# Kernel optimization log

Hardware: AMD Instinct MI355X
Metric: run time of the kernel (lower is better)

## Reference

```python
import jax, jax.numpy as jnp
import numpy as np
from jax.scipy.special import logsumexp

B, D, A = 64, 128, 128


def setup_inputs() -> dict:
    key = jax.random.key(0)
    k1, k2, k3, k4 = jax.random.split(key, 4)
    x = jax.random.randint(k1, (B, D), 0, 2).astype(jnp.float32)  # binary observations
    u_log_p_a1 = jax.random.normal(k2, (1, 1, 1, A), dtype=jnp.float32)
    u_log_transition = jax.random.normal(k3, (D - 1, A, A), dtype=jnp.float32)
    log_p_xi_g_ai = jax.random.normal(k4, (1, D, 1, A), dtype=jnp.float32)
    return {
        "x": x,
        "u_log_p_a1": u_log_p_a1,
        "u_log_transition": u_log_transition,
        "log_p_xi_g_ai": log_p_xi_g_ai,
    }


def reference(x, u_log_p_a1, u_log_transition, log_p_xi_g_ai):
    b, d = x.shape
    a = u_log_p_a1.shape[-1]
    # _normalize_logits == log_softmax along last dim
    log_p_a1 = jax.nn.log_softmax(u_log_p_a1, axis=-1)          # [1,1,1,A]
    log_T = jax.nn.log_softmax(u_log_transition, axis=-1)        # [D-1,A,A]
    # Bernoulli(logits=l).log_prob(v) = v*l - softplus(l)
    l = log_p_xi_g_ai                                            # [1,D,1,A]
    log_px_vec = x[:, :, None, None] * l - jax.nn.softplus(l)    # [B,D,1,A]
    # per-step reduction matrices
    red = log_px_vec[:, 1:] + log_T                              # [B,D-1,A,A]
    # initial matrix: row-repeated initial vector
    init = jnp.broadcast_to(log_px_vec[:, 0] + log_p_a1[0], (b, a, a))  # [B,A,A]
    mats = jnp.transpose(red, (1, 0, 2, 3))                      # [D-1,B,A,A]

    def step(M, T):
        # log-space matmul: new[b,i,j] = logsumexp_k M[b,i,k] + T[b,k,j]
        new = logsumexp(M[:, :, :, None] + T[:, None, :, :], axis=2)
        return new, None

    final, _ = jax.lax.scan(step, init, mats)                    # [B,A,A]
    log_px = logsumexp(final, axis=-1)                           # [B,A] (rows identical)
    return (log_px, log_p_a1)
```

## Files before the change

kernel.cpp:

```cpp
#include <hip/hip_runtime.h>


#define B_ 64
#define D_ 128
#define A_ 128
#define T_ 127

#define E16_UINTS (T_ * 8192)
#define BC_OFF E16_UINTS
#define BC_SZ (B_ * T_ * A_)
#define LP_OFF (BC_OFF + BC_SZ)

typedef _Float16 h2 __attribute__((ext_vector_type(2)));

__device__ __forceinline__ int packrtz(float a, float b) {
    auto p = __builtin_amdgcn_cvt_pkrtz(a, b);
    return __builtin_bit_cast(int, p);
}
__device__ __forceinline__ float dot2acc(unsigned int e, unsigned int s, float acc) {
    return __builtin_amdgcn_fdot2(__builtin_bit_cast(h2, e),
                                  __builtin_bit_cast(h2, s), acc, false);
}

template <int CTRL>
__device__ __forceinline__ float dpp_mov_self(float x) {
    return __int_as_float(__builtin_amdgcn_update_dpp(
        __float_as_int(x), __float_as_int(x), CTRL, 0xF, 0xF, false));
}
template <int CTRL>
__device__ __forceinline__ float dpp_mov_zero(float x) {
    return __int_as_float(__builtin_amdgcn_update_dpp(
        0, __float_as_int(x), CTRL, 0xF, 0xF, true));
}
__device__ __forceinline__ float wave_max_bcast(float x) {
    x = fmaxf(x, dpp_mov_self<0x111>(x));
    x = fmaxf(x, dpp_mov_self<0x112>(x));
    x = fmaxf(x, dpp_mov_self<0x114>(x));
    x = fmaxf(x, dpp_mov_self<0x118>(x));
    x = fmaxf(x, dpp_mov_self<0x142>(x));
    x = fmaxf(x, dpp_mov_self<0x143>(x));
    return __int_as_float(__builtin_amdgcn_readlane(__float_as_int(x), 63));
}
__device__ __forceinline__ float wave_sum_bcast(float x) {
    x += dpp_mov_zero<0x111>(x);
    x += dpp_mov_zero<0x112>(x);
    x += dpp_mov_zero<0x114>(x);
    x += dpp_mov_zero<0x118>(x);
    x += dpp_mov_zero<0x142>(x);
    x += dpp_mov_zero<0x143>(x);
    return __int_as_float(__builtin_amdgcn_readlane(__float_as_int(x), 63));
}

__global__ __launch_bounds__(256) void prep(const float* __restrict__ uT,
                                            const float* __restrict__ u1,
                                            const float* __restrict__ x,
                                            const float* __restrict__ lg,
                                            float* __restrict__ ws,
                                            float* __restrict__ out) {
    __shared__ float Zl[A_];
    const int t = blockIdx.x, tid = threadIdx.x;
    const int wave = tid >> 6, lane = tid & 63;
    const float* u = uT + (size_t)t * A_ * A_;

    for (int rr = 0; rr < 32; rr++) {
        int r = wave * 32 + rr;
        float a = u[r * A_ + lane];
        float c = u[r * A_ + lane + 64];
        float mx = wave_max_bcast(fmaxf(a, c));
        float s = wave_sum_bcast(__expf(a - mx) + __expf(c - mx));
        if (lane == 0) Zl[r] = mx + __logf(s);
    }
    __syncthreads();

    unsigned int* Et = (unsigned int*)ws + (size_t)t * 8192;
    for (int it = 0; it < 32; it++) {
        int a = it * 256 + tid;
        int c = a & 3, jl = (a >> 2) & 31, w = (a >> 7) & 3;
        int h = (a >> 9) & 1, q = (a >> 10) & 7;
        int j = 32 * w + jl;
        int i = 32 * h + 4 * q + c;
        float e0 = __expf(u[(2 * i) * A_ + j] - Zl[2 * i]);
        float e1 = __expf(u[(2 * i + 1) * A_ + j] - Zl[2 * i + 1]);
        Et[a] = (unsigned int)packrtz(e0, e1);
    }

    {
        int j = tid & 127, hb = tid >> 7;
        float lv = lg[(t + 1) * A_ + j];
        float sp = (lv > 0.f) ? (lv + log1pf(__expf(-lv))) : log1pf(__expf(lv));
        float g0 = -sp, g1 = lv - sp;
        float* BC = ws + BC_OFF;
        for (int b = hb * 32; b < hb * 32 + 32; b++) {
            float xv = x[b * D_ + t + 1];
            BC[((size_t)b * T_ + t) * A_ + j] = (xv != 0.f) ? g1 : g0;
        }
    }

    if (t == 0 && wave == 0) {
        float a = u1[lane], c = u1[lane + 64];
        float mx = wave_max_bcast(fmaxf(a, c));
        float s = wave_sum_bcast(__expf(a - mx) + __expf(c - mx));
        float lse = mx + __logf(s);
        ws[LP_OFF + lane] = a - lse;
        ws[LP_OFF + lane + 64] = c - lse;
        out[B_ * A_ + lane] = a - lse;
        out[B_ * A_ + lane + 64] = c - lse;
    }
}

#define BARRIER() asm volatile("s_waitcnt lgkmcnt(0)\n\ts_barrier" ::: "memory")

#define STEP(T, EC, EP, BCC, BCP, DOPF)                                       \
    {                                                                         \
        const int p = (T) & 1, np = p ^ 1;                                    \
        if (DOPF) {                \
            const uint4* pf = (const uint4*)(Eb + (size_t)((T) + 2) * 32768); \
            _Pragma("unroll") for (int q = 0; q < 8; q++) EP[q] = pf[q * 256];\
            BCP = BCg[((T) + 2) * A_];                                       \
            __builtin_amdgcn_sched_barrier(0);  \
        }                                                                     \
        float4 vm4 = *(const float4*)&vmaxl[p][0];                            \
        const uint4* ewp = (const uint4*)&ewl[p][0] + h * 8;                  \
        uint4 ew_[8];                                                         \
        _Pragma("unroll") for (int q = 0; q < 8; q++) ew_[q] = ewp[q];        \
        float vA = h ? vm4.z : vm4.x;                                         \
        float vB = h ? vm4.w : vm4.y;                                         \
        float m = fmaxf(fmaxf(vm4.x, vm4.y), fmaxf(vm4.z, vm4.w));            \
        float fA = __expf(vA - m), fB = __expf(vB - m);                       \
        float s0 = 0, s1 = 0, s2 = 0, s3 = 0;                                 \
        float r0 = 0, r1 = 0, r2 = 0, r3 = 0;                                 \
        _Pragma("unroll") for (int q = 0; q < 4; q++) {                       \
            s0 = dot2acc(EC[q].x, ew_[q].x, s0);                              \
            s1 = dot2acc(EC[q].y, ew_[q].y, s1);                              \
            s2 = dot2acc(EC[q].z, ew_[q].z, s2);                              \
            s3 = dot2acc(EC[q].w, ew_[q].w, s3);                              \
        }                                                                     \
        _Pragma("unroll") for (int q = 4; q < 8; q++) {                       \
            r0 = dot2acc(EC[q].x, ew_[q].x, r0);                              \
            r1 = dot2acc(EC[q].y, ew_[q].y, r1);                              \
            r2 = dot2acc(EC[q].z, ew_[q].z, r2);                              \
            r3 = dot2acc(EC[q].w, ew_[q].w, r3);                              \
        }                                                                     \
        float S = ((s0 + s1) + (s2 + s3)) * fA + ((r0 + r1) + (r2 + r3)) * fB;\
        S += __shfl_xor(S, 32, 64);                                           \
        float vnew = __logf(S) + m + BCC;                                     \
        float mw2 = wave_max_bcast(vnew);                                     \
        ewl[np][j] = (_Float16)__expf(vnew - mw2);                            \
        vmaxl[np][w] = mw2;                                                   \
        v = vnew;                                                             \
        BARRIER();                                                            \
    }

__global__ __launch_bounds__(256, 1) void fwd(const float* __restrict__ x,
                                              const float* __restrict__ lg,
                                              const float* __restrict__ ws,
                                              float* __restrict__ out) {
    __shared__ __align__(16) _Float16 ewl[2][A_];
    __shared__ __align__(16) float vmaxl[2][4];
    __shared__ float sums[4];
    const int b = blockIdx.x, tid = threadIdx.x;
    const int w = tid >> 6, lane = tid & 63;
    const int h = lane >> 5, jl = lane & 31;
    const int j = 32 * w + jl;

    const char* Eb = (const char*)ws + (size_t)h * 2048 + w * 512 + jl * 16;
    const float* BCg = ws + BC_OFF + (size_t)b * T_ * A_ + j;
    const float* LP = ws + LP_OFF;

    float ll = lg[j];
    float sp = (ll > 0.f) ? (ll + log1pf(__expf(-ll))) : log1pf(__expf(ll));
    float xv0 = x[b * D_];
    float v = LP[j] + ((xv0 != 0.f) ? (ll - sp) : (-sp));
    float mw = wave_max_bcast(v);
    ewl[0][j] = (_Float16)__expf(v - mw);
    vmaxl[0][w] = mw;

    uint4 E0[8], E1[8], E2[8];
    float bc0, bc1, bc2;
    {
        const uint4* p0 = (const uint4*)(Eb);
        const uint4* p1 = (const uint4*)(Eb + 32768);
#pragma unroll
        for (int q = 0; q < 8; q++) { E0[q] = p0[q * 256]; E1[q] = p1[q * 256]; }
        bc0 = BCg[0];
        bc1 = BCg[A_];
        __builtin_amdgcn_sched_barrier(0);
    }
    bc2 = 0.f;
    BARRIER();

    for (int t = 0; t < 123; t += 3) {
        STEP(t + 0, E0, E2, bc0, bc2, 1)
        STEP(t + 1, E1, E0, bc1, bc0, 1)
        STEP(t + 2, E2, E1, bc2, bc1, 1)
    }
    STEP(123, E0, E2, bc0, bc2, 1)
    STEP(124, E1, E0, bc1, bc0, 1)
    STEP(125, E2, E1, bc2, bc1, 0)
    STEP(126, E0, E1, bc0, bc1, 0)

    float4 vmf = *(const float4*)&vmaxl[1][0];
    float mf = fmaxf(fmaxf(vmf.x, vmf.y), fmaxf(vmf.z, vmf.w));
    float sw = wave_sum_bcast(__expf(v - mf)) * 0.5f;
    sums[w] = sw;
    BARRIER();
    float tot = (sums[0] + sums[1]) + (sums[2] + sums[3]);
    float L = mf + __logf(tot);
    if (tid < A_) out[b * A_ + tid] = L;
}

extern "C" void kernel_launch(void* const* d_in, const int* in_sizes, int n_in,
                              void* d_out, int out_size, void* d_ws, size_t ws_size,
                              hipStream_t stream) {
    const float* x = (const float*)d_in[0];
    const float* u1 = (const float*)d_in[1];
    const float* uT = (const float*)d_in[2];
    const float* lg = (const float*)d_in[3];
    float* ws = (float*)d_ws;
    float* out = (float*)d_out;

    prep<<<dim3(T_), dim3(256), 0, stream>>>(uT, u1, x, lg, ws, out);
    fwd<<<dim3(B_), dim3(256), 0, stream>>>(x, lg, ws, out);
}
```

Measured before the change: 158.6 us.

## Shrink forward block to two waves with lagged max normalization

The sequential forward kernel drops from 256 to 128 threads, so each thread owns one output column and does the full 128-length dot product itself. This removes the cross-half shuffle and the per-step broadcast of the wave max, and normalizes with the previous step's max. The prep kernel now stages each transition matrix in shared memory and computes row log-normalizers per thread, and the E layout is re-packed to match. It trades more per-thread work and doubled register prefetch for fewer waves, fewer sync steps per iteration, and a shorter dependency chain, with some risk of fp16 underflow from the stale max.

```diff
diff --git a/kernel.cpp b/kernel.cpp
--- a/kernel.cpp
+++ b/kernel.cpp
@@ -13,13 +13,13 @@
 
 typedef _Float16 h2 __attribute__((ext_vector_type(2)));
 
+__device__ __forceinline__ float dot2acc(unsigned int e, unsigned int s, float acc) {
+    return __builtin_amdgcn_fdot2(__builtin_bit_cast(h2, e),
+                                  __builtin_bit_cast(h2, s), acc, false);
+}
 __device__ __forceinline__ int packrtz(float a, float b) {
     auto p = __builtin_amdgcn_cvt_pkrtz(a, b);
     return __builtin_bit_cast(int, p);
-}
-__device__ __forceinline__ float dot2acc(unsigned int e, unsigned int s, float acc) {
-    return __builtin_amdgcn_fdot2(__builtin_bit_cast(h2, e),
-                                  __builtin_bit_cast(h2, s), acc, false);
 }
 
 template <int CTRL>
@@ -32,14 +32,18 @@
     return __int_as_float(__builtin_amdgcn_update_dpp(
         0, __float_as_int(x), CTRL, 0xF, 0xF, true));
 }
-__device__ __forceinline__ float wave_max_bcast(float x) {
+__device__ __forceinline__ float wave_max_partial(float x) {
     x = fmaxf(x, dpp_mov_self<0x111>(x));
     x = fmaxf(x, dpp_mov_self<0x112>(x));
     x = fmaxf(x, dpp_mov_self<0x114>(x));
     x = fmaxf(x, dpp_mov_self<0x118>(x));
     x = fmaxf(x, dpp_mov_self<0x142>(x));
     x = fmaxf(x, dpp_mov_self<0x143>(x));
-    return __int_as_float(__builtin_amdgcn_readlane(__float_as_int(x), 63));
+    return x;
+}
+__device__ __forceinline__ float wave_max_bcast(float x) {
+    return __int_as_float(__builtin_amdgcn_readlane(
+        __float_as_int(wave_max_partial(x)), 63));
 }
 __device__ __forceinline__ float wave_sum_bcast(float x) {
     x += dpp_mov_zero<0x111>(x);
@@ -57,30 +61,34 @@
                                             const float* __restrict__ lg,
                                             float* __restrict__ ws,
                                             float* __restrict__ out) {
-    __shared__ float Zl[A_];
+    __shared__ float ul[128 * 128];
     const int t = blockIdx.x, tid = threadIdx.x;
-    const int wave = tid >> 6, lane = tid & 63;
     const float* u = uT + (size_t)t * A_ * A_;
 
-    for (int rr = 0; rr < 32; rr++) {
-        int r = wave * 32 + rr;
-        float a = u[r * A_ + lane];
-        float c = u[r * A_ + lane + 64];
-        float mx = wave_max_bcast(fmaxf(a, c));
-        float s = wave_sum_bcast(__expf(a - mx) + __expf(c - mx));
-        if (lane == 0) Zl[r] = mx + __logf(s);
+    for (int i = tid; i < 4096; i += 256) {
+        float4 v4 = ((const float4*)u)[i];
+        *(float4*)&ul[(i >> 5) * 128 + (i & 31) * 4] = v4;
+    }
+    __syncthreads();
+
+    if (tid < 128) {
+        const int r = tid;
+        float mx = -1e30f;
+        for (int it = 0; it < 128; it++) mx = fmaxf(mx, ul[r * 128 + ((it + r) & 127)]);
+        float s = 0.f;
+        for (int it = 0; it < 128; it++) s += __expf(ul[r * 128 + ((it + r) & 127)] - mx);
+        float Z = mx + __logf(s);
+        for (int it = 0; it < 128; it++) ul[r * 128 + ((it + r) & 127)] -= Z;
     }
     __syncthreads();
 
     unsigned int* Et = (unsigned int*)ws + (size_t)t * 8192;
     for (int it = 0; it < 32; it++) {
         int a = it * 256 + tid;
-        int c = a & 3, jl = (a >> 2) & 31, w = (a >> 7) & 3;
-        int h = (a >> 9) & 1, q = (a >> 10) & 7;
-        int j = 32 * w + jl;
-        int i = 32 * h + 4 * q + c;
-        float e0 = __expf(u[(2 * i) * A_ + j] - Zl[2 * i]);
-        float e1 = __expf(u[(2 * i + 1) * A_ + j] - Zl[2 * i + 1]);
+        int c = a & 3, j = (a >> 2) & 127, q = a >> 9;
+        int i = 4 * q + c;
+        float e0 = __expf(ul[(2 * i) * 128 + j]);
+        float e1 = __expf(ul[(2 * i + 1) * 128 + j]);
         Et[a] = (unsigned int)packrtz(e0, e1);
     }
 
@@ -96,7 +104,8 @@
         }
     }
 
-    if (t == 0 && wave == 0) {
+    if (t == 0 && tid < 64) {
+        int lane = tid;
         float a = u1[lane], c = u1[lane + 64];
         float mx = wave_max_bcast(fmaxf(a, c));
         float s = wave_sum_bcast(__expf(a - mx) + __expf(c - mx));
@@ -113,57 +122,45 @@
 #define STEP(T, EC, EP, BCC, BCP, DOPF)                                       \
     {                                                                         \
         const int p = (T) & 1, np = p ^ 1;                                    \
-        if (DOPF) {                \
-            const uint4* pf = (const uint4*)(Eb + (size_t)((T) + 2) * 32768); \
-            _Pragma("unroll") for (int q = 0; q < 8; q++) EP[q] = pf[q * 256];\
-            BCP = BCg[((T) + 2) * A_];                                       \
-            __builtin_amdgcn_sched_barrier(0);  \
+        if (DOPF) {                                    \
+            const uint4* pfp = (const uint4*)(Eb + (size_t)((T) + 1) * 32768);\
+            _Pragma("unroll") for (int q = 0; q < 16; q++) EP[q] = pfp[q*128];\
+            BCP = BCg[((T) + 1) * A_];                                        \
+            __builtin_amdgcn_sched_barrier(0);                                \
         }                                                                     \
-        float4 vm4 = *(const float4*)&vmaxl[p][0];                            \
-        const uint4* ewp = (const uint4*)&ewl[p][0] + h * 8;                  \
-        uint4 ew_[8];                                                         \
-        _Pragma("unroll") for (int q = 0; q < 8; q++) ew_[q] = ewp[q];        \
-        float vA = h ? vm4.z : vm4.x;                                         \
-        float vB = h ? vm4.w : vm4.y;                                         \
-        float m = fmaxf(fmaxf(vm4.x, vm4.y), fmaxf(vm4.z, vm4.w));            \
-        float fA = __expf(vA - m), fB = __expf(vB - m);                       \
-        float s0 = 0, s1 = 0, s2 = 0, s3 = 0;                                 \
-        float r0 = 0, r1 = 0, r2 = 0, r3 = 0;                                 \
-        _Pragma("unroll") for (int q = 0; q < 4; q++) {                       \
-            s0 = dot2acc(EC[q].x, ew_[q].x, s0);                              \
-            s1 = dot2acc(EC[q].y, ew_[q].y, s1);                              \
-            s2 = dot2acc(EC[q].z, ew_[q].z, s2);                              \
-            s3 = dot2acc(EC[q].w, ew_[q].w, s3);                              \
+        float2 vm2 = *(const float2*)&vml[p][0];                              \
+        float Mcur = fmaxf(vm2.x, vm2.y);                                     \
+        const uint4* ewp = (const uint4*)&ewl[p][0];                          \
+        float a0 = 0, a1 = 0, a2 = 0, a3 = 0;                                 \
+        _Pragma("unroll") for (int q = 0; q < 16; q++) {                      \
+            uint4 e = ewp[q];                                                 \
+            a0 = dot2acc(EC[q].x, e.x, a0);                                   \
+            a1 = dot2acc(EC[q].y, e.y, a1);                                   \
+            a2 = dot2acc(EC[q].z, e.z, a2);                                   \
+            a3 = dot2acc(EC[q].w, e.w, a3);                                   \
         }                                                                     \
-        _Pragma("unroll") for (int q = 4; q < 8; q++) {                       \
-            r0 = dot2acc(EC[q].x, ew_[q].x, r0);                              \
-            r1 = dot2acc(EC[q].y, ew_[q].y, r1);                              \
-            r2 = dot2acc(EC[q].z, ew_[q].z, r2);                              \
-            r3 = dot2acc(EC[q].w, ew_[q].w, r3);                              \
-        }                                                                     \
-        float S = ((s0 + s1) + (s2 + s3)) * fA + ((r0 + r1) + (r2 + r3)) * fB;\
-        S += __shfl_xor(S, 32, 64);                                           \
-        float vnew = __logf(S) + m + BCC;                                     \
-        float mw2 = wave_max_bcast(vnew);                                     \
-        ewl[np][j] = (_Float16)__expf(vnew - mw2);                            \
-        vmaxl[np][w] = mw2;                                                   \
+        float S = (a0 + a1) + (a2 + a3);                                      \
+        float vnew = __logf(S) + Mp + BCC;                                    \
+        ewl[np][j] = (_Float16)__expf(vnew - Mcur);   \
+        float wm = wave_max_partial(vnew);             \
+        if (lane == 63) vml[np][w] = wm;                                      \
         v = vnew;                                                             \
+        Mp = Mcur;                                                            \
         BARRIER();                                                            \
     }
 
-__global__ __launch_bounds__(256, 1) void fwd(const float* __restrict__ x,
-                                              const float* __restrict__ lg,
-                                              const float* __restrict__ ws,
-                                              float* __restrict__ out) {
+__global__ __launch_bounds__(128) void fwd(const float* __restrict__ x,
+                                           const float* __restrict__ lg,
+                                           const float* __restrict__ ws,
+                                           float* __restrict__ out) {
     __shared__ __align__(16) _Float16 ewl[2][A_];
-    __shared__ __align__(16) float vmaxl[2][4];
-    __shared__ float sums[4];
+    __shared__ float vml[2][2];
+    __shared__ float sums[2];
     const int b = blockIdx.x, tid = threadIdx.x;
     const int w = tid >> 6, lane = tid & 63;
-    const int h = lane >> 5, jl = lane & 31;
-    const int j = 32 * w + jl;
-
-    const char* Eb = (const char*)ws + (size_t)h * 2048 + w * 512 + jl * 16;
+    const int j = 64 * w + lane;
+
+    const char* Eb = (const char*)ws + j * 16;
     const float* BCg = ws + BC_OFF + (size_t)b * T_ * A_ + j;
     const float* LP = ws + LP_OFF;
 
@@ -171,42 +168,36 @@
     float sp = (ll > 0.f) ? (ll + log1pf(__expf(-ll))) : log1pf(__expf(ll));
     float xv0 = x[b * D_];
     float v = LP[j] + ((xv0 != 0.f) ? (ll - sp) : (-sp));
-    float mw = wave_max_bcast(v);
-    ewl[0][j] = (_Float16)__expf(v - mw);
-    vmaxl[0][w] = mw;
-
-    uint4 E0[8], E1[8], E2[8];
-    float bc0, bc1, bc2;
+    float wm0 = wave_max_bcast(v);
+    if (lane == 0) vml[0][w] = wm0;
+    BARRIER();
+    float Mp = fmaxf(vml[0][0], vml[0][1]);
+    ewl[0][j] = (_Float16)__expf(v - Mp);
+
+    uint4 E0[16], E1[16];
+    float bc0, bc1;
     {
         const uint4* p0 = (const uint4*)(Eb);
-        const uint4* p1 = (const uint4*)(Eb + 32768);
 #pragma unroll
-        for (int q = 0; q < 8; q++) { E0[q] = p0[q * 256]; E1[q] = p1[q * 256]; }
+        for (int q = 0; q < 16; q++) E0[q] = p0[q * 128];
         bc0 = BCg[0];
-        bc1 = BCg[A_];
         __builtin_amdgcn_sched_barrier(0);
     }
-    bc2 = 0.f;
+    bc1 = 0.f;
     BARRIER();
 
-    for (int t = 0; t < 123; t += 3) {
-        STEP(t + 0, E0, E2, bc0, bc2, 1)
+    for (int t = 0; t < 126; t += 2) {
+        STEP(t + 0, E0, E1, bc0, bc1, 1)
         STEP(t + 1, E1, E0, bc1, bc0, 1)
-        STEP(t + 2, E2, E1, bc2, bc1, 1)
-    }
-    STEP(123, E0, E2, bc0, bc2, 1)
-    STEP(124, E1, E0, bc1, bc0, 1)
-    STEP(125, E2, E1, bc2, bc1, 0)
+    }
     STEP(126, E0, E1, bc0, bc1, 0)
 
-    float4 vmf = *(const float4*)&vmaxl[1][0];
-    float mf = fmaxf(fmaxf(vmf.x, vmf.y), fmaxf(vmf.z, vmf.w));
-    float sw = wave_sum_bcast(__expf(v - mf)) * 0.5f;
-    sums[w] = sw;
+    float Mf = fmaxf(vml[1][0], vml[1][1]);
+    float sw = wave_sum_bcast(__expf(v - Mf));
+    if (lane == 0) sums[w] = sw;
     BARRIER();
-    float tot = (sums[0] + sums[1]) + (sums[2] + sums[3]);
-    float L = mf + __logf(tot);
-    if (tid < A_) out[b * A_ + tid] = L;
+    float L = Mf + __logf(sums[0] + sums[1]);
+    out[b * A_ + j] = L;
 }
 
 extern "C" void kernel_launch(void* const* d_in, const int* in_sizes, int n_in,
@@ -220,5 +211,5 @@
     float* out = (float*)d_out;
 
     prep<<<dim3(T_), dim3(256), 0, stream>>>(uT, u1, x, lg, ws, out);
-    fwd<<<dim3(B_), dim3(256), 0, stream>>>(x, lg, ws, out);
-}
+    fwd<<<dim3(B_), dim3(128), 0, stream>>>(x, lg, ws, out);
+}
```

Result: slower. 177.1 us (+11.6%).
